# Performance work log

Measured on AMD Instinct MI355X. Metric: run time of the kernel, lower is better.

## Reference

```python
import jax, jax.numpy as jnp
import numpy as np

B, S, H, L = 4, 2048, 1024, 4
EPS = 1e-5
NEG = -1e9


def setup_inputs() -> dict:
    key = jax.random.key(0)
    ks = jax.random.split(key, 10)
    scale = 1.0 / np.sqrt(H)
    inp = {
        "x": jax.random.normal(ks[0], (B, S, H), dtype=jnp.float32),
        "mask": jnp.ones((B, 1, S), dtype=jnp.int32),
        # stacked per-layer params; torch Linear weight is [out, in]
        "Wq": jax.random.normal(ks[1], (L, H, H), dtype=jnp.float32) * scale,
        "bq": jnp.zeros((L, H), dtype=jnp.float32),
        "Wk": jax.random.normal(ks[2], (L, H, H), dtype=jnp.float32) * scale,
        "bk": jnp.zeros((L, H), dtype=jnp.float32),
        "Wv": jax.random.normal(ks[3], (L, H, H), dtype=jnp.float32) * scale,
        "bv": jnp.zeros((L, H), dtype=jnp.float32),
        "ln_w": jnp.ones((L, H), dtype=jnp.float32),
        "ln_b": jnp.zeros((L, H), dtype=jnp.float32),
    }
    return inp


def _layer(x, mask0, Wq, bq, Wk, bk, Wv, bv, ln_w, ln_b):
    # torch Linear: y = x @ W^T + b
    q = jnp.einsum("bsh,oh->bso", x, Wq) + bq
    k = jnp.einsum("bsh,oh->bso", x, Wk) + bk
    v = jnp.einsum("bsh,oh->bso", x, Wv) + bv
    inv_sqrt_h = jnp.asarray(1.0 / np.sqrt(H), x.dtype)
    scores = jnp.einsum("bsh,bth->bst", q, k) * inv_sqrt_h  # [B,S,S]
    scores = jnp.where(mask0, jnp.asarray(NEG, x.dtype), scores)
    probs = jax.nn.softmax(scores, axis=-1)
    attn = jnp.einsum("bst,bth->bsh", probs, v)
    # residual + LayerNorm (dropout is identity at eval)
    y = x + attn
    mu = jnp.mean(y, axis=-1, keepdims=True)
    var = jnp.mean(jnp.square(y - mu), axis=-1, keepdims=True)
    return ln_w * (y - mu) * jax.lax.rsqrt(var + EPS) + ln_b


def reference(x, mask, Wq, bq, Wk, bk, Wv, bv, ln_w, ln_b):
    mask0 = (mask == 0)  # [B,1,S], broadcasts over query dim
    for l in range(Wq.shape[0]):
        x = _layer(x, mask0, Wq[l], bq[l], Wk[l], bk[l], Wv[l], bv[l], ln_w[l], ln_b[l])
    return x
```

## Files before the change

### kernel.cpp

```cpp
#include <hip/hip_runtime.h>
#include <stdint.h>

typedef __bf16 bf16_t;
typedef __bf16 bf16x8 __attribute__((ext_vector_type(8)));
typedef __bf16 bf16x4 __attribute__((ext_vector_type(4)));
typedef float f32x4 __attribute__((ext_vector_type(4)));
typedef float f32x16 __attribute__((ext_vector_type(16)));
typedef unsigned int u32;

#define DEVINL static __device__ __forceinline__

constexpr int BB = 4;
constexpr int SEQ = 2048;
constexpr int HID = 1024;
constexpr int NL = 4;
constexpr int MR = BB * SEQ;
constexpr float LN_EPS = 1e-5f;

DEVINL f32x4 mfma16(bf16x8 a, bf16x8 b, f32x4 c) {
  return __builtin_amdgcn_mfma_f32_16x16x32_bf16(a, b, c, 0, 0, 0);
}
DEVINL f32x16 mfma32(bf16x8 a, bf16x8 b, f32x16 c) {
  return __builtin_amdgcn_mfma_f32_32x32x16_bf16(a, b, c, 0, 0, 0);
}

DEVINL void gload_lds16(const bf16_t* g, bf16_t* l) {
  __builtin_amdgcn_global_load_lds(
      (const __attribute__((address_space(1))) u32*)g,
      (__attribute__((address_space(3))) u32*)l, 16, 0, 0);
}

__global__ __launch_bounds__(512, 2) void gemm_qkv(
    const bf16_t* __restrict__ xb, const bf16_t* __restrict__ w0,
    const bf16_t* __restrict__ w1, const bf16_t* __restrict__ w2,
    const float* __restrict__ bias0, const float* __restrict__ bias1,
    const float* __restrict__ bias2, bf16_t* __restrict__ o0,
    bf16_t* __restrict__ o1, bf16_t* __restrict__ vT) {
  constexpr int BM = 256, BN = 128, NT = 16;

  __shared__ bf16_t smem[2 * BM * 64 + 2 * BN * 64];
  bf16_t* lA = smem;
  bf16_t* lB = smem + 2 * BM * 64;

  const int nwg = gridDim.x;
  int Lb = blockIdx.x;
  Lb = (Lb & 7) * (nwg >> 3) + (Lb >> 3);
  const int z = Lb >> 8;
  const int rem = Lb & 255;
  const int tm = rem >> 3;
  const int tn = rem & 7;
  const int brow = tm * BM, bcol = tn * BN;

  const bf16_t* B = (z == 0) ? w0 : (z == 1) ? w1 : w2;
  const float* bias = (z == 0) ? bias0 : (z == 1) ? bias1 : bias2;

  const int t = threadIdx.x, wave = t >> 6, lane = t & 63;
  const int wm = wave >> 1, wn = wave & 1;
  const int r31 = lane & 31, kb2 = lane >> 5;
  const int srow = t >> 3;
  const int cbk = (t & 7) ^ (srow & 7);
  const bf16_t* pAs = xb + (size_t)(brow + srow) * HID + cbk * 8;
  const bf16_t* pBs = B + (size_t)(bcol + srow) * HID + cbk * 8;
  bf16_t* lAw = lA + wave * 512;
  bf16_t* lBw = lB + wave * 512;

#define SA(X_, h_)                                                  \
  gload_lds16(pAs + (size_t)((h_)*64) * HID + (X_)*64,              \
              lAw + ((X_)&1) * (BM * 64) + (h_)*4096)
#define SB(X_, h_)                                                  \
  gload_lds16(pBs + (size_t)((h_)*64) * HID + (X_)*64,              \
              lBw + ((X_)&1) * (BN * 64) + (h_)*4096)

  const char* lAc = (const char*)lA;
  const char* lBc = (const char*)lB;
  int sX[4];
#pragma unroll
  for (int ks = 0; ks < 4; ++ks) sX[ks] = (((ks * 2 + kb2) ^ (r31 & 7)) << 4);
  const int rowA0 = wm * 64 + r31;
  const int rowB0 = wn * 64 + r31;

  f32x16 acc00 = {}, acc01 = {}, acc10 = {}, acc11 = {};

  SA(0, 0); SA(0, 1); SA(0, 2); SA(0, 3);
  SB(0, 0); SB(0, 1);
  SB(1, 0); SB(1, 1);
  asm volatile("s_waitcnt vmcnt(2)" ::: "memory");
  __builtin_amdgcn_s_barrier();

  for (int kt = 0; kt < NT; ++kt) {
    const char* aB = lAc + (kt & 1) * (BM * 128);
    const char* bB = lBc + (kt & 1) * (BN * 128);
    bf16x8 bF[2][4], a0[4];
#pragma unroll
    for (int ni = 0; ni < 2; ++ni)
#pragma unroll
      for (int ks = 0; ks < 4; ++ks)
        bF[ni][ks] = *(const bf16x8*)(bB + (rowB0 + ni * 32) * 128 + sX[ks]);
#pragma unroll
    for (int ks = 0; ks < 4; ++ks)
      a0[ks] = *(const bf16x8*)(aB + rowA0 * 128 + sX[ks]);
    if (kt + 1 < NT) { SA(kt + 1, 0); SA(kt + 1, 1); SA(kt + 1, 2); SA(kt + 1, 3); }
    __builtin_amdgcn_s_barrier();
    __builtin_amdgcn_s_setprio(1);
#pragma unroll
    for (int ks = 0; ks < 4; ++ks) {
      acc00 = mfma32(a0[ks], bF[0][ks], acc00);
      acc01 = mfma32(a0[ks], bF[1][ks], acc01);
    }
    __builtin_amdgcn_s_setprio(0);
    __builtin_amdgcn_s_barrier();
    bf16x8 a1[4];
#pragma unroll
    for (int ks = 0; ks < 4; ++ks)
      a1[ks] = *(const bf16x8*)(aB + (rowA0 + 32) * 128 + sX[ks]);
    if (kt + 2 < NT) { SB(kt + 2, 0); SB(kt + 2, 1); }
    __builtin_amdgcn_s_barrier();
    __builtin_amdgcn_s_setprio(1);
#pragma unroll
    for (int ks = 0; ks < 4; ++ks) {
      acc10 = mfma32(a1[ks], bF[0][ks], acc10);
      acc11 = mfma32(a1[ks], bF[1][ks], acc11);
    }
    __builtin_amdgcn_s_setprio(0);
    if (kt < NT - 2)
      asm volatile("s_waitcnt vmcnt(2)" ::: "memory");
    else
      asm volatile("s_waitcnt vmcnt(0)" ::: "memory");
    __builtin_amdgcn_s_barrier();
  }

  if (z < 2) {
    const int crow = brow + wm * 64 + 4 * kb2;
    const int ccol = bcol + wn * 64 + r31;
    bf16_t* outb = (z == 0) ? o0 : o1;
#pragma unroll
    for (int mi = 0; mi < 2; ++mi) {
#pragma unroll
      for (int ni = 0; ni < 2; ++ni) {
        const f32x16 av = (mi == 0) ? (ni == 0 ? acc00 : acc01)
                                    : (ni == 0 ? acc10 : acc11);
        const int col = ccol + ni * 32;
        const float badd = bias[col];
#pragma unroll
        for (int r = 0; r < 16; ++r) {
          const int row = crow + mi * 32 + (r & 3) + 8 * (r >> 2);
          outb[(size_t)row * HID + col] = (bf16_t)(av[r] + badd);
        }
      }
    }
  } else {
    bf16_t* tp = smem + wave * (64 * 72);
#pragma unroll
    for (int mi = 0; mi < 2; ++mi) {
#pragma unroll
      for (int ni = 0; ni < 2; ++ni) {
        const f32x16 av = (mi == 0) ? (ni == 0 ? acc00 : acc01)
                                    : (ni == 0 ? acc10 : acc11);
        const int cl = r31 + ni * 32;
        const float badd = bias[bcol + wn * 64 + cl];
#pragma unroll
        for (int g = 0; g < 4; ++g) {
          const int rl = mi * 32 + 8 * g + 4 * kb2;
          bf16x4 ov;
#pragma unroll
          for (int i = 0; i < 4; ++i) ov[i] = (bf16_t)(av[4 * g + i] + badd);
          *(bf16x4*)(tp + cl * 72 + rl) = ov;
        }
      }
    }
    asm volatile("s_waitcnt lgkmcnt(0)" ::: "memory");
    const int batch = brow >> 11;
    bf16_t* vt = vT + (size_t)batch * HID * SEQ;
    const int c0 = bcol + wn * 64;
    const int s0 = (brow & 2047) + wm * 64;
    const int lr = lane >> 3, lc = (lane & 7) * 8;
#pragma unroll
    for (int p = 0; p < 8; ++p) {
      const int rt = p * 8 + lr;
      const bf16x8 vv = *(const bf16x8*)(tp + rt * 72 + lc);
      *(bf16x8*)(vt + (size_t)(c0 + rt) * SEQ + s0 + lc) = vv;
    }
  }
#undef SA
#undef SB
}

template <int EPI>
__global__ __launch_bounds__(512, 2) void gemm8(
    const bf16_t* __restrict__ Ab, const bf16_t* __restrict__ B0,
    const int* __restrict__ maskp, float* __restrict__ rsum,
    bf16_t* __restrict__ o0, bf16_t* __restrict__ o1) {
  constexpr int TM = 8;
  constexpr int TN = (EPI == 1) ? 8 : 4;
  constexpr int LDA = (EPI == 2) ? SEQ : HID;
  constexpr int LDB = (EPI == 2) ? SEQ : HID;
  constexpr int LDC = (EPI == 1) ? SEQ : HID;
  constexpr int NT = 16;

  __shared__ bf16_t lA[2 * 16384];
  __shared__ bf16_t lB[2 * 16384];

  const int nwg = gridDim.x;
  int Lb = blockIdx.x;
  Lb = (Lb & 7) * (nwg >> 3) + (Lb >> 3);
  const int z = Lb / (TM * TN);
  const int rem = Lb - z * (TM * TN);
  const int tm = rem / TN;
  const int tn = rem - tm * TN;
  const int brow = tm * 256, bcol = tn * 256;

  const bf16_t* A;
  const bf16_t* B;
  bf16_t* outb;
  int zb = 0;
  if (EPI == 1) {
    A = Ab + (size_t)z * SEQ * HID;
    B = B0 + (size_t)z * SEQ * HID;
    outb = o0 + (size_t)z * SEQ * SEQ;
  } else {
    zb = z >> 1;
    const int kh = z & 1;
    A = Ab + (size_t)zb * SEQ * SEQ + kh * 1024;
    B = B0 + (size_t)zb * HID * SEQ + kh * 1024;
    outb = ((kh == 0) ? o0 : o1) + (size_t)zb * SEQ * HID;
  }

  const int t = threadIdx.x, wave = t >> 6, lane = t & 63;
  const int wm = wave >> 2, wn = wave & 3;
  const int fr = lane & 15, kb = lane >> 4;
  const int srow = t >> 3;
  const int cbk = (t & 7) ^ (srow & 7);
  const bf16_t* pAs = A + (size_t)(brow + srow) * LDA + cbk * 8;
  const bf16_t* pBs = B + (size_t)(bcol + srow) * LDB + cbk * 8;
  bf16_t* lAw = lA + wave * 512;
  bf16_t* lBw = lB + wave * 512;

#define SA(X_, h_)                                                  \
  gload_lds16(pAs + (size_t)((h_)*64) * LDA + (X_)*64,              \
              lAw + ((X_)&1) * 16384 + (h_)*4096)
#define SB(X_, h_)                                                  \
  gload_lds16(pBs + (size_t)((h_)*64) * LDB + (X_)*64,              \
              lBw + ((X_)&1) * 16384 + (h_)*4096)

  const char* lAc = (const char*)lA;
  const char* lBc = (const char*)lB;
  const int cX0 = ((kb ^ (fr & 7)) << 4);
  const int cX1 = cX0 ^ 64;
  const int bRowOff = (wn & 1) * 64;

  f32x4 acc[8][4] = {};

  SA(0, 0); SA(0, 1); SA(0, 2); SA(0, 3);
  SB(0, 0); SB(0, 1); SB(0, 2); SB(0, 3);
  SA(1, 0); SA(1, 2);
  SB(1, 0); SB(1, 1); SB(1, 2); SB(1, 3);
  asm volatile("s_waitcnt vmcnt(6)" ::: "memory");
  __builtin_amdgcn_s_barrier();

  for (int kt = 0; kt < NT; ++kt) {
    const char* aB = lAc + (kt & 1) * 32768 + wm * 16384;
    const char* bB = lBc + (kt & 1) * 32768 + (wn >> 1) * 16384;
    bf16x8 bf_[4][2];
#pragma unroll
    for (int p = 0; p < 4; ++p) {
      if (p == 0) {
#pragma unroll
        for (int n = 0; n < 4; ++n) {
          const int rb = (bRowOff + n * 16 + fr) * 128;
          bf_[n][0] = *(const bf16x8*)(bB + rb + cX0);
          bf_[n][1] = *(const bf16x8*)(bB + rb + cX1);
        }
      }
      const int ra0 = (p * 32 + fr) * 128;
      const int ra1 = (p * 32 + 16 + fr) * 128;
      bf16x8 a00 = *(const bf16x8*)(aB + ra0 + cX0);
      bf16x8 a01 = *(const bf16x8*)(aB + ra0 + cX1);
      bf16x8 a10 = *(const bf16x8*)(aB + ra1 + cX0);
      bf16x8 a11 = *(const bf16x8*)(aB + ra1 + cX1);
      if (p == 0 && kt + 1 < NT) { SA(kt + 1, 1); SA(kt + 1, 3); }
      if (p == 1 && kt + 2 < NT) { SB(kt + 2, 0); SB(kt + 2, 1); }
      if (p == 2 && kt + 2 < NT) { SA(kt + 2, 0); SA(kt + 2, 2); }
      if (p == 3 && kt + 2 < NT) { SB(kt + 2, 2); SB(kt + 2, 3); }
      __builtin_amdgcn_s_barrier();
      __builtin_amdgcn_s_setprio(1);
#pragma unroll
      for (int n = 0; n < 4; ++n) {
        acc[2 * p][n] = mfma16(a00, bf_[n][0], acc[2 * p][n]);
        acc[2 * p][n] = mfma16(a01, bf_[n][1], acc[2 * p][n]);
        acc[2 * p + 1][n] = mfma16(a10, bf_[n][0], acc[2 * p + 1][n]);
        acc[2 * p + 1][n] = mfma16(a11, bf_[n][1], acc[2 * p + 1][n]);
      }
      __builtin_amdgcn_s_setprio(0);
      if (p == 3) {
        if (kt < NT - 3)
          asm volatile("s_waitcnt vmcnt(6)" ::: "memory");
        else
          asm volatile("s_waitcnt vmcnt(0)" ::: "memory");
      }
      __builtin_amdgcn_s_barrier();
    }
  }

  const int qr = lane >> 4;
  const int crow = brow + wm * 128 + qr * 4;
  const int ccol = bcol + wn * 64 + fr;
  if (EPI == 1) {
    const int* mrow = maskp + (size_t)z * SEQ;
    float* rs = rsum + (size_t)z * SEQ;
    int mv[4];
#pragma unroll
    for (int n = 0; n < 4; ++n) mv[n] = mrow[ccol + n * 16];
#pragma unroll
    for (int m = 0; m < 8; ++m) {
      const int row = crow + m * 16;
#pragma unroll
      for (int j = 0; j < 4; ++j) {
        float rp = 0.f;
#pragma unroll
        for (int n = 0; n < 4; ++n) {
          const int col = ccol + n * 16;
          const float p = mv[n] ? __expf(acc[m][n][j] * 0.03125f) : 0.f;
          outb[(size_t)(row + j) * LDC + col] = (bf16_t)p;
          rp += p;
        }
        rp += __shfl_xor(rp, 1, 64);
        rp += __shfl_xor(rp, 2, 64);
        rp += __shfl_xor(rp, 4, 64);
        rp += __shfl_xor(rp, 8, 64);
        if (fr == 0) atomicAdd(&rs[row + j], rp);
      }
    }
  } else {
    const float* rv = rsum + (size_t)zb * SEQ;
#pragma unroll
    for (int m = 0; m < 8; ++m) {
      const int row = crow + m * 16;
#pragma unroll
      for (int j = 0; j < 4; ++j) {
        const float ri = 1.f / rv[row + j];
#pragma unroll
        for (int n = 0; n < 4; ++n) {
          const int col = ccol + n * 16;
          outb[(size_t)(row + j) * LDC + col] = (bf16_t)(acc[m][n][j] * ri);
        }
      }
    }
  }
#undef SA
#undef SB
}

__global__ __launch_bounds__(256) void cast4(
    const float* __restrict__ s0, const float* __restrict__ s1,
    const float* __restrict__ s2, const float* __restrict__ s3,
    bf16_t* __restrict__ d0, bf16_t* __restrict__ d1,
    bf16_t* __restrict__ d2, bf16_t* __restrict__ d3, long nW4, long nX4) {
  const int y = blockIdx.y;
  const float* in = (y == 0) ? s0 : (y == 1) ? s1 : (y == 2) ? s2 : s3;
  bf16_t* out = (y == 0) ? d0 : (y == 1) ? d1 : (y == 2) ? d2 : d3;
  const long n4 = (y == 3) ? nX4 : nW4;
  const long stride = (long)gridDim.x * blockDim.x;
  for (long i = (long)blockIdx.x * blockDim.x + threadIdx.x; i < n4;
       i += stride) {
    f32x4 x = *(const f32x4*)(in + i * 4);
    bf16x4 o;
#pragma unroll
    for (int j = 0; j < 4; ++j) o[j] = (bf16_t)x[j];
    *(bf16x4*)(out + i * 4) = o;
  }
}

__global__ __launch_bounds__(256) void resid_ln(
    const bf16_t* __restrict__ part0, const bf16_t* __restrict__ part1,
    const float* __restrict__ xinf, const bf16_t* __restrict__ xinb,
    const float* __restrict__ lnw, const float* __restrict__ lnb,
    float* __restrict__ xout, bf16_t* __restrict__ xbout) {
  const int row = blockIdx.x;
  const int t = threadIdx.x;
  const int wave = t >> 6;
  const int lane = t & 63;
  const size_t base = (size_t)row * HID + t * 4;
  const bf16x4 a0 = *(const bf16x4*)(part0 + base);
  const bf16x4 a1 = *(const bf16x4*)(part1 + base);
  f32x4 xv;
  if (xinf != nullptr) {
    xv = *(const f32x4*)(xinf + base);
  } else {
    const bf16x4 xbv = *(const bf16x4*)(xinb + base);
#pragma unroll
    for (int j = 0; j < 4; ++j) xv[j] = (float)xbv[j];
  }
  f32x4 y;
#pragma unroll
  for (int j = 0; j < 4; ++j) y[j] = (float)a0[j] + (float)a1[j] + xv[j];
  float s1 = y[0] + y[1] + y[2] + y[3];
  float s2 = y[0] * y[0] + y[1] * y[1] + y[2] * y[2] + y[3] * y[3];
#pragma unroll
  for (int off = 32; off > 0; off >>= 1) {
    s1 += __shfl_xor(s1, off, 64);
    s2 += __shfl_xor(s2, off, 64);
  }
  __shared__ float red[8];
  if (lane == 0) {
    red[wave] = s1;
    red[4 + wave] = s2;
  }
  __syncthreads();
  s1 = red[0] + red[1] + red[2] + red[3];
  s2 = red[4] + red[5] + red[6] + red[7];
  const float mu = s1 * (1.f / HID);
  const float var = s2 * (1.f / HID) - mu * mu;
  const float rs = rsqrtf(var + LN_EPS);
  const f32x4 wv = *(const f32x4*)(lnw + t * 4);
  const f32x4 bv = *(const f32x4*)(lnb + t * 4);
  f32x4 o;
#pragma unroll
  for (int j = 0; j < 4; ++j) o[j] = wv[j] * ((y[j] - mu) * rs) + bv[j];
  if (xout != nullptr) *(f32x4*)(xout + base) = o;
  if (xbout != nullptr) {
    bf16x4 ob;
#pragma unroll
    for (int j = 0; j < 4; ++j) ob[j] = (bf16_t)o[j];
    *(bf16x4*)(xbout + base) = ob;
  }
}

extern "C" void kernel_launch(void* const* d_in, const int* in_sizes, int n_in,
                              void* d_out, int out_size, void* d_ws,
                              size_t ws_size, hipStream_t stream) {
  const float* x_in = (const float*)d_in[0];
  const int* mask = (const int*)d_in[1];
  const float* Wq = (const float*)d_in[2];
  const float* bq = (const float*)d_in[3];
  const float* Wk = (const float*)d_in[4];
  const float* bk = (const float*)d_in[5];
  const float* Wv = (const float*)d_in[6];
  const float* bv = (const float*)d_in[7];
  const float* lnw = (const float*)d_in[8];
  const float* lnb = (const float*)d_in[9];
  float* out = (float*)d_out;

  char* ws = (char*)d_ws;
  size_t off = 0;
  auto alloc = [&](size_t bytes) {
    char* p = ws + off;
    off += (bytes + 255) & ~(size_t)255;
    return (void*)p;
  };
  const size_t LHH = (size_t)NL * HID * HID;
  bf16_t* wqb = (bf16_t*)alloc(LHH * 2);
  bf16_t* wkb = (bf16_t*)alloc(LHH * 2);
  bf16_t* wvb = (bf16_t*)alloc(LHH * 2);
  bf16_t* xb = (bf16_t*)alloc((size_t)MR * HID * 2);
  bf16_t* q = (bf16_t*)alloc((size_t)MR * HID * 2);
  bf16_t* k = (bf16_t*)alloc((size_t)MR * HID * 2);
  bf16_t* vT = (bf16_t*)alloc((size_t)MR * HID * 2);
  bf16_t* scores = (bf16_t*)alloc((size_t)BB * SEQ * SEQ * 2);
  bf16_t* attn0 = (bf16_t*)alloc((size_t)MR * HID * 2);
  bf16_t* attn1 = (bf16_t*)alloc((size_t)MR * HID * 2);
  float* rsum = (float*)alloc((size_t)MR * 4);
  if (off > ws_size) return;

  cast4<<<dim3(1024, 4), 256, 0, stream>>>(Wq, Wk, Wv, x_in, wqb, wkb, wvb, xb,
                                           (long)(LHH / 4),
                                           (long)((size_t)MR * HID / 4));

  for (int l = 0; l < NL; ++l) {
    const size_t wo = (size_t)l * HID * HID;
    gemm_qkv<<<768, 512, 0, stream>>>(xb, wqb + wo, wkb + wo, wvb + wo,
                                      bq + (size_t)l * HID,
                                      bk + (size_t)l * HID,
                                      bv + (size_t)l * HID, q, k, vT);
    hipMemsetAsync(rsum, 0, (size_t)MR * 4, stream);
    gemm8<1><<<256, 512, 0, stream>>>(q, k, mask, rsum, scores, nullptr);
    gemm8<2><<<256, 512, 0, stream>>>(scores, vT, nullptr, rsum, attn0, attn1);
    const float* xif = (l == 0) ? x_in : nullptr;
    float* xo = (l == NL - 1) ? out : nullptr;
    bf16_t* xbo = (l == NL - 1) ? nullptr : xb;
    resid_ln<<<MR, 256, 0, stream>>>(attn0, attn1, xif, xb,
                                     lnw + (size_t)l * HID,
                                     lnb + (size_t)l * HID, xo, xbo);
  }
}
```

Baseline: 656.7 us.

## Replace split-K PV GEMM with dedicated full-K 256x128 tile kernel

The probs·V GEMM used to split K into two halves, each written to its own bf16 partial buffer, and the residual+LayerNorm kernel summed them. A new gemm_pv kernel now runs the full K=2048 reduction per 256x128 output tile using 32x32x16 MFMAs and a double-buffered LDS pipeline. The result goes to a single attention buffer. This removes one partial-output write and read and the extra add in resid_ln, and avoids rounding the partials to bf16 twice. In exchange the K loop per workgroup is longer and the tile is narrower, so more of the scores matrix is re-read per output column.

```diff
diff --git a/kernel.cpp b/kernel.cpp
--- a/kernel.cpp
+++ b/kernel.cpp
@@ -185,17 +185,129 @@
 #undef SB
 }
 
-template <int EPI>
-__global__ __launch_bounds__(512, 2) void gemm8(
+__global__ __launch_bounds__(512, 2) void gemm_pv(
+    const bf16_t* __restrict__ scores, const bf16_t* __restrict__ vT,
+    const float* __restrict__ rsum, bf16_t* __restrict__ attn) {
+  constexpr int BM = 256, BN = 128, NT = 32;
+
+  __shared__ bf16_t smem[2 * BM * 64 + 2 * BN * 64];
+  bf16_t* lA = smem;
+  bf16_t* lB = smem + 2 * BM * 64;
+
+  const int nwg = gridDim.x;
+  int Lb = blockIdx.x;
+  Lb = (Lb & 7) * (nwg >> 3) + (Lb >> 3);
+  const int z = Lb >> 6;
+  const int rem = Lb & 63;
+  const int tm = rem >> 3;
+  const int tn = rem & 7;
+  const int brow = tm * BM, bcol = tn * BN;
+
+  const bf16_t* A = scores + (size_t)z * SEQ * SEQ;
+  const bf16_t* B = vT + (size_t)z * HID * SEQ;
+  bf16_t* outb = attn + (size_t)z * SEQ * HID;
+
+  const int t = threadIdx.x, wave = t >> 6, lane = t & 63;
+  const int wm = wave >> 1, wn = wave & 1;
+  const int r31 = lane & 31, kb2 = lane >> 5;
+  const int srow = t >> 3;
+  const int cbk = (t & 7) ^ (srow & 7);
+  const bf16_t* pAs = A + (size_t)(brow + srow) * SEQ + cbk * 8;
+  const bf16_t* pBs = B + (size_t)(bcol + srow) * SEQ + cbk * 8;
+  bf16_t* lAw = lA + wave * 512;
+  bf16_t* lBw = lB + wave * 512;
+
+#define SA(X_, h_)                                                  \
+  gload_lds16(pAs + (size_t)((h_)*64) * SEQ + (X_)*64,              \
+              lAw + ((X_)&1) * (BM * 64) + (h_)*4096)
+#define SB(X_, h_)                                                  \
+  gload_lds16(pBs + (size_t)((h_)*64) * SEQ + (X_)*64,              \
+              lBw + ((X_)&1) * (BN * 64) + (h_)*4096)
+
+  const char* lAc = (const char*)lA;
+  const char* lBc = (const char*)lB;
+  int sX[4];
+#pragma unroll
+  for (int ks = 0; ks < 4; ++ks) sX[ks] = (((ks * 2 + kb2) ^ (r31 & 7)) << 4);
+  const int rowA0 = wm * 64 + r31;
+  const int rowB0 = wn * 64 + r31;
+
+  f32x16 acc00 = {}, acc01 = {}, acc10 = {}, acc11 = {};
+
+  SA(0, 0); SA(0, 1); SA(0, 2); SA(0, 3);
+  SB(0, 0); SB(0, 1);
+  SB(1, 0); SB(1, 1);
+  asm volatile("s_waitcnt vmcnt(2)" ::: "memory");
+  __builtin_amdgcn_s_barrier();
+
+  for (int kt = 0; kt < NT; ++kt) {
+    const char* aB = lAc + (kt & 1) * (BM * 128);
+    const char* bB = lBc + (kt & 1) * (BN * 128);
+    bf16x8 bF[2][4], a0[4];
+#pragma unroll
+    for (int ni = 0; ni < 2; ++ni)
+#pragma unroll
+      for (int ks = 0; ks < 4; ++ks)
+        bF[ni][ks] = *(const bf16x8*)(bB + (rowB0 + ni * 32) * 128 + sX[ks]);
+#pragma unroll
+    for (int ks = 0; ks < 4; ++ks)
+      a0[ks] = *(const bf16x8*)(aB + rowA0 * 128 + sX[ks]);
+    if (kt + 1 < NT) { SA(kt + 1, 0); SA(kt + 1, 1); SA(kt + 1, 2); SA(kt + 1, 3); }
+    __builtin_amdgcn_s_barrier();
+    __builtin_amdgcn_s_setprio(1);
+#pragma unroll
+    for (int ks = 0; ks < 4; ++ks) {
+      acc00 = mfma32(a0[ks], bF[0][ks], acc00);
+      acc01 = mfma32(a0[ks], bF[1][ks], acc01);
+    }
+    __builtin_amdgcn_s_setprio(0);
+    __builtin_amdgcn_s_barrier();
+    bf16x8 a1[4];
+#pragma unroll
+    for (int ks = 0; ks < 4; ++ks)
+      a1[ks] = *(const bf16x8*)(aB + (rowA0 + 32) * 128 + sX[ks]);
+    if (kt + 2 < NT) { SB(kt + 2, 0); SB(kt + 2, 1); }
+    __builtin_amdgcn_s_barrier();
+    __builtin_amdgcn_s_setprio(1);
+#pragma unroll
+    for (int ks = 0; ks < 4; ++ks) {
+      acc10 = mfma32(a1[ks], bF[0][ks], acc10);
+      acc11 = mfma32(a1[ks], bF[1][ks], acc11);
+    }
+    __builtin_amdgcn_s_setprio(0);
+    if (kt < NT - 2)
+      asm volatile("s_waitcnt vmcnt(2)" ::: "memory");
+    else
+      asm volatile("s_waitcnt vmcnt(0)" ::: "memory");
+    __builtin_amdgcn_s_barrier();
+  }
+
+  const float* rv = rsum + (size_t)z * SEQ;
+  const int crow = brow + wm * 64 + 4 * kb2;
+  const int ccol = bcol + wn * 64 + r31;
+#pragma unroll
+  for (int mi = 0; mi < 2; ++mi) {
+#pragma unroll
+    for (int ni = 0; ni < 2; ++ni) {
+      const f32x16 av = (mi == 0) ? (ni == 0 ? acc00 : acc01)
+                                  : (ni == 0 ? acc10 : acc11);
+      const int col = ccol + ni * 32;
+#pragma unroll
+      for (int r = 0; r < 16; ++r) {
+        const int row = crow + mi * 32 + (r & 3) + 8 * (r >> 2);
+        outb[(size_t)row * HID + col] = (bf16_t)(av[r] / rv[row]);
+      }
+    }
+  }
+#undef SA
+#undef SB
+}
+
+__global__ __launch_bounds__(512, 2) void gemm_qk(
     const bf16_t* __restrict__ Ab, const bf16_t* __restrict__ B0,
     const int* __restrict__ maskp, float* __restrict__ rsum,
-    bf16_t* __restrict__ o0, bf16_t* __restrict__ o1) {
-  constexpr int TM = 8;
-  constexpr int TN = (EPI == 1) ? 8 : 4;
-  constexpr int LDA = (EPI == 2) ? SEQ : HID;
-  constexpr int LDB = (EPI == 2) ? SEQ : HID;
-  constexpr int LDC = (EPI == 1) ? SEQ : HID;
-  constexpr int NT = 16;
+    bf16_t* __restrict__ o0) {
+  constexpr int TM = 8, TN = 8, NT = 16;
 
   __shared__ bf16_t lA[2 * 16384];
   __shared__ bf16_t lB[2 * 16384];
@@ -209,37 +321,25 @@
   const int tn = rem - tm * TN;
   const int brow = tm * 256, bcol = tn * 256;
 
-  const bf16_t* A;
-  const bf16_t* B;
-  bf16_t* outb;
-  int zb = 0;
-  if (EPI == 1) {
-    A = Ab + (size_t)z * SEQ * HID;
-    B = B0 + (size_t)z * SEQ * HID;
-    outb = o0 + (size_t)z * SEQ * SEQ;
-  } else {
-    zb = z >> 1;
-    const int kh = z & 1;
-    A = Ab + (size_t)zb * SEQ * SEQ + kh * 1024;
-    B = B0 + (size_t)zb * HID * SEQ + kh * 1024;
-    outb = ((kh == 0) ? o0 : o1) + (size_t)zb * SEQ * HID;
-  }
+  const bf16_t* A = Ab + (size_t)z * SEQ * HID;
+  const bf16_t* B = B0 + (size_t)z * SEQ * HID;
+  bf16_t* outb = o0 + (size_t)z * SEQ * SEQ;
 
   const int t = threadIdx.x, wave = t >> 6, lane = t & 63;
   const int wm = wave >> 2, wn = wave & 3;
   const int fr = lane & 15, kb = lane >> 4;
   const int srow = t >> 3;
   const int cbk = (t & 7) ^ (srow & 7);
-  const bf16_t* pAs = A + (size_t)(brow + srow) * LDA + cbk * 8;
-  const bf16_t* pBs = B + (size_t)(bcol + srow) * LDB + cbk * 8;
+  const bf16_t* pAs = A + (size_t)(brow + srow) * HID + cbk * 8;
+  const bf16_t* pBs = B + (size_t)(bcol + srow) * HID + cbk * 8;
   bf16_t* lAw = lA + wave * 512;
   bf16_t* lBw = lB + wave * 512;
 
 #define SA(X_, h_)                                                  \
-  gload_lds16(pAs + (size_t)((h_)*64) * LDA + (X_)*64,              \
+  gload_lds16(pAs + (size_t)((h_)*64) * HID + (X_)*64,              \
               lAw + ((X_)&1) * 16384 + (h_)*4096)
 #define SB(X_, h_)                                                  \
-  gload_lds16(pBs + (size_t)((h_)*64) * LDB + (X_)*64,              \
+  gload_lds16(pBs + (size_t)((h_)*64) * HID + (X_)*64,              \
               lBw + ((X_)&1) * 16384 + (h_)*4096)
 
   const char* lAc = (const char*)lA;
@@ -304,46 +404,29 @@
   const int qr = lane >> 4;
   const int crow = brow + wm * 128 + qr * 4;
   const int ccol = bcol + wn * 64 + fr;
-  if (EPI == 1) {
-    const int* mrow = maskp + (size_t)z * SEQ;
-    float* rs = rsum + (size_t)z * SEQ;
-    int mv[4];
-#pragma unroll
-    for (int n = 0; n < 4; ++n) mv[n] = mrow[ccol + n * 16];
-#pragma unroll
-    for (int m = 0; m < 8; ++m) {
-      const int row = crow + m * 16;
-#pragma unroll
-      for (int j = 0; j < 4; ++j) {
-        float rp = 0.f;
-#pragma unroll
-        for (int n = 0; n < 4; ++n) {
-          const int col = ccol + n * 16;
-          const float p = mv[n] ? __expf(acc[m][n][j] * 0.03125f) : 0.f;
-          outb[(size_t)(row + j) * LDC + col] = (bf16_t)p;
-          rp += p;
-        }
-        rp += __shfl_xor(rp, 1, 64);
-        rp += __shfl_xor(rp, 2, 64);
-        rp += __shfl_xor(rp, 4, 64);
-        rp += __shfl_xor(rp, 8, 64);
-        if (fr == 0) atomicAdd(&rs[row + j], rp);
-      }
-    }
-  } else {
-    const float* rv = rsum + (size_t)zb * SEQ;
-#pragma unroll
-    for (int m = 0; m < 8; ++m) {
-      const int row = crow + m * 16;
-#pragma unroll
-      for (int j = 0; j < 4; ++j) {
-        const float ri = 1.f / rv[row + j];
-#pragma unroll
-        for (int n = 0; n < 4; ++n) {
-          const int col = ccol + n * 16;
-          outb[(size_t)(row + j) * LDC + col] = (bf16_t)(acc[m][n][j] * ri);
-        }
-      }
+  const int* mrow = maskp + (size_t)z * SEQ;
+  float* rs = rsum + (size_t)z * SEQ;
+  int mv[4];
+#pragma unroll
+  for (int n = 0; n < 4; ++n) mv[n] = mrow[ccol + n * 16];
+#pragma unroll
+  for (int m = 0; m < 8; ++m) {
+    const int row = crow + m * 16;
+#pragma unroll
+    for (int j = 0; j < 4; ++j) {
+      float rp = 0.f;
+#pragma unroll
+      for (int n = 0; n < 4; ++n) {
+        const int col = ccol + n * 16;
+        const float p = mv[n] ? __expf(acc[m][n][j] * 0.03125f) : 0.f;
+        outb[(size_t)(row + j) * SEQ + col] = (bf16_t)p;
+        rp += p;
+      }
+      rp += __shfl_xor(rp, 1, 64);
+      rp += __shfl_xor(rp, 2, 64);
+      rp += __shfl_xor(rp, 4, 64);
+      rp += __shfl_xor(rp, 8, 64);
+      if (fr == 0) atomicAdd(&rs[row + j], rp);
     }
   }
 #undef SA
@@ -371,17 +454,16 @@
 }
 
 __global__ __launch_bounds__(256) void resid_ln(
-    const bf16_t* __restrict__ part0, const bf16_t* __restrict__ part1,
-    const float* __restrict__ xinf, const bf16_t* __restrict__ xinb,
-    const float* __restrict__ lnw, const float* __restrict__ lnb,
-    float* __restrict__ xout, bf16_t* __restrict__ xbout) {
+    const bf16_t* __restrict__ part0, const float* __restrict__ xinf,
+    const bf16_t* __restrict__ xinb, const float* __restrict__ lnw,
+    const float* __restrict__ lnb, float* __restrict__ xout,
+    bf16_t* __restrict__ xbout) {
   const int row = blockIdx.x;
   const int t = threadIdx.x;
   const int wave = t >> 6;
   const int lane = t & 63;
   const size_t base = (size_t)row * HID + t * 4;
   const bf16x4 a0 = *(const bf16x4*)(part0 + base);
-  const bf16x4 a1 = *(const bf16x4*)(part1 + base);
   f32x4 xv;
   if (xinf != nullptr) {
     xv = *(const f32x4*)(xinf + base);
@@ -392,7 +474,7 @@
   }
   f32x4 y;
 #pragma unroll
-  for (int j = 0; j < 4; ++j) y[j] = (float)a0[j] + (float)a1[j] + xv[j];
+  for (int j = 0; j < 4; ++j) y[j] = (float)a0[j] + xv[j];
   float s1 = y[0] + y[1] + y[2] + y[3];
   float s2 = y[0] * y[0] + y[1] * y[1] + y[2] * y[2] + y[3] * y[3];
 #pragma unroll
@@ -456,8 +538,7 @@
   bf16_t* k = (bf16_t*)alloc((size_t)MR * HID * 2);
   bf16_t* vT = (bf16_t*)alloc((size_t)MR * HID * 2);
   bf16_t* scores = (bf16_t*)alloc((size_t)BB * SEQ * SEQ * 2);
-  bf16_t* attn0 = (bf16_t*)alloc((size_t)MR * HID * 2);
-  bf16_t* attn1 = (bf16_t*)alloc((size_t)MR * HID * 2);
+  bf16_t* attn = (bf16_t*)alloc((size_t)MR * HID * 2);
   float* rsum = (float*)alloc((size_t)MR * 4);
   if (off > ws_size) return;
 
@@ -472,13 +553,12 @@
                                       bk + (size_t)l * HID,
                                       bv + (size_t)l * HID, q, k, vT);
     hipMemsetAsync(rsum, 0, (size_t)MR * 4, stream);
-    gemm8<1><<<256, 512, 0, stream>>>(q, k, mask, rsum, scores, nullptr);
-    gemm8<2><<<256, 512, 0, stream>>>(scores, vT, nullptr, rsum, attn0, attn1);
+    gemm_qk<<<256, 512, 0, stream>>>(q, k, mask, rsum, scores);
+    gemm_pv<<<256, 512, 0, stream>>>(scores, vT, rsum, attn);
     const float* xif = (l == 0) ? x_in : nullptr;
     float* xo = (l == NL - 1) ? out : nullptr;
     bf16_t* xbo = (l == NL - 1) ? nullptr : xb;
-    resid_ln<<<MR, 256, 0, stream>>>(attn0, attn1, xif, xb,
-                                     lnw + (size_t)l * HID,
+    resid_ln<<<MR, 256, 0, stream>>>(attn, xif, xb, lnw + (size_t)l * HID,
                                      lnb + (size_t)l * HID, xo, xbo);
   }
 }
```

Result: no change. 664.5 us (+1.2%).
